# Optimization experiments

Hardware: AMD Instinct MI355X
Metric: run time of the kernel (lower is better)

The kernel has to match this reference:

```python
import jax, jax.numpy as jnp
import numpy as np

HIDDEN = 768
INTER = 2048
N_EXPERTS = 8
TOP_K = 2
SWIGLU_LIMIT = 7.0
N_TOK = 8192


def setup_inputs() -> dict:
    key = jax.random.key(0)
    k_x, k_r, k_gu, k_d = jax.random.split(key, 4)
    x = jax.random.normal(k_x, (N_TOK, HIDDEN), dtype=jnp.float32)
    router_w = jax.random.normal(k_r, (N_EXPERTS, HIDDEN), dtype=jnp.float32) * 0.02
    gate_up_proj = jax.random.normal(k_gu, (N_EXPERTS, 2 * INTER, HIDDEN), dtype=jnp.float32) * 0.02
    down_proj = jax.random.normal(k_d, (N_EXPERTS, HIDDEN, INTER), dtype=jnp.float32) * 0.02
    return {"x": x, "router_w": router_w, "gate_up_proj": gate_up_proj, "down_proj": down_proj}


def reference(x, router_w, gate_up_proj, down_proj):
    # router: [n_tok, E]
    router_logits = x @ router_w.T
    topk_vals, topk_idx = jax.lax.top_k(router_logits, TOP_K)  # [n_tok, k]
    topk_weights = jax.nn.softmax(topk_vals.astype(jnp.float32), axis=-1).astype(x.dtype)

    out = jnp.zeros_like(x)
    # Loop over the small fixed expert set; each expert is a dense GEMM over all
    # tokens, masked by its per-token routing weight (0 for unrouted tokens) —
    # identical math to the original gather/GEMM/scatter dispatch.
    for e in range(N_EXPERTS):
        # per-token weight for expert e (sums slots; each expert appears at most once per token)
        w_e = jnp.sum(jnp.where(topk_idx == e, topk_weights, 0.0), axis=-1)  # [n_tok]
        gate_up = x @ gate_up_proj[e].T  # [n_tok, 2*I]
        gate, up = jnp.split(gate_up, 2, axis=-1)
        up = jnp.minimum(up, SWIGLU_LIMIT)
        mlp_out = (jax.nn.silu(gate) * up) @ down_proj[e].T  # [n_tok, H]
        out = out + mlp_out * w_e[:, None]
    return out
```

## Files before the change

### kernel.cpp

```cpp
#include <hip/hip_runtime.h>
#include <hip/hip_bf16.h>

typedef unsigned short u16;
typedef unsigned int u32;
typedef short bf16x8 __attribute__((ext_vector_type(8)));
typedef float f32x4 __attribute__((ext_vector_type(4)));

#define NTOK 8192
#define HID 768
#define INTER 2048
#define NEXP 8

#define MFMA16(a, b, c) __builtin_amdgcn_mfma_f32_16x16x32_bf16(a, b, c, 0, 0, 0)
#define S_BARRIER() __builtin_amdgcn_s_barrier()
#define SETPRIO(x) __builtin_amdgcn_s_setprio(x)
#define WAITVM(n) asm volatile("s_waitcnt vmcnt(" #n ")" ::: "memory")

__device__ __forceinline__ u16 f2bf(float f) {
    u32 u = __builtin_bit_cast(u32, f);
    u32 r = (u + 0x7FFFu + ((u >> 16) & 1u)) >> 16;
    return (u16)r;
}

__device__ __forceinline__ void gld16(const void* g, void* l) {
    __builtin_amdgcn_global_load_lds((const __attribute__((address_space(1))) void*)g,
                                     (__attribute__((address_space(3))) void*)l, 16, 0, 0);
}

__global__ __launch_bounds__(256) void zero_kernel(float4* out4, int n4) {
    int i = blockIdx.x * blockDim.x + threadIdx.x;
    float4 z = {0.f, 0.f, 0.f, 0.f};
    int stride = gridDim.x * blockDim.x;
    for (int k = i; k < n4; k += stride) out4[k] = z;
}

__global__ __launch_bounds__(256) void cvt_kernel(const float* __restrict__ src, u16* __restrict__ dst, int n8) {
    int i = blockIdx.x * blockDim.x + threadIdx.x;
    int stride = gridDim.x * blockDim.x;
    for (; i < n8; i += stride) {
        const float4* s = (const float4*)(src + (size_t)i * 8);
        float4 a = s[0], b = s[1];
        u16 r[8] = {f2bf(a.x), f2bf(a.y), f2bf(a.z), f2bf(a.w),
                    f2bf(b.x), f2bf(b.y), f2bf(b.z), f2bf(b.w)};
        *(uint4*)(dst + (size_t)i * 8) = *(const uint4*)r;
    }
}

__global__ __launch_bounds__(256) void router2(const float* __restrict__ x, const float* __restrict__ rw,
                                               u32* __restrict__ route, float* __restrict__ wslot) {
    int wv = threadIdx.x >> 6, ln = threadIdx.x & 63;
    int t = blockIdx.x * 4 + wv;
    if (t >= NTOK) return;
    float xr[12];
#pragma unroll
    for (int j = 0; j < 12; j++) xr[j] = x[(size_t)t * HID + ln + j * 64];
    float lg[NEXP];
#pragma unroll
    for (int e = 0; e < NEXP; e++) {
        float a = 0.f;
#pragma unroll
        for (int j = 0; j < 12; j++) a += xr[j] * rw[e * HID + ln + j * 64];
#pragma unroll
        for (int off = 32; off; off >>= 1) a += __shfl_xor(a, off);
        lg[e] = a;
    }
    int i0 = 0;
    float v0 = lg[0];
#pragma unroll
    for (int e = 1; e < NEXP; e++)
        if (lg[e] > v0) { v0 = lg[e]; i0 = e; }
    int i1 = -1;
    float v1 = -1e30f;
#pragma unroll
    for (int e = 0; e < NEXP; e++) {
        if (e == i0) continue;
        if (lg[e] > v1) { v1 = lg[e]; i1 = e; }
    }
    float w0 = 1.f / (1.f + __expf(v1 - v0));
    float w1 = 1.f - w0;
    if (ln == 0) {
        wslot[0 * NTOK + t] = w0;
        wslot[1 * NTOK + t] = w1;
        route[t] = (u32)i0 | ((u32)i1 << 8);
    }
}

__global__ __launch_bounds__(1024) void scatter_kernel(const u32* __restrict__ route, int* __restrict__ counts,
                                                       int* __restrict__ tokslot, int* __restrict__ ntiles,
                                                       int* __restrict__ tiledesc) {
    __shared__ int sc[NEXP][1024];
    int tid = threadIdx.x;
    u32 rt[8];
    int cnt[NEXP] = {0, 0, 0, 0, 0, 0, 0, 0};
#pragma unroll
    for (int k = 0; k < 8; k++) {
        rt[k] = route[tid * 8 + k];
        cnt[rt[k] & 255]++;
        cnt[(rt[k] >> 8) & 255]++;
    }
#pragma unroll
    for (int e = 0; e < NEXP; e++) sc[e][tid] = cnt[e];
    __syncthreads();
    for (int off = 1; off < 1024; off <<= 1) {
        int v[NEXP];
#pragma unroll
        for (int e = 0; e < NEXP; e++) v[e] = (tid >= off) ? sc[e][tid - off] : 0;
        __syncthreads();
#pragma unroll
        for (int e = 0; e < NEXP; e++)
            if (tid >= off) sc[e][tid] += v[e];
        __syncthreads();
    }
    int base[NEXP];
#pragma unroll
    for (int e = 0; e < NEXP; e++) base[e] = sc[e][tid] - cnt[e];
#pragma unroll
    for (int k = 0; k < 8; k++) {
        int t = tid * 8 + k;
        int e0 = rt[k] & 255, e1 = (rt[k] >> 8) & 255;
        tokslot[e0 * NTOK + base[e0]] = t;
        base[e0]++;
        tokslot[e1 * NTOK + base[e1]] = t | (1 << 16);
        base[e1]++;
    }
    if (tid == 0) {
        int tot = 0;
        for (int e = 0; e < NEXP; e++) {
            int c = sc[e][1023];
            counts[e] = c;
            int nt = (c + 255) >> 8;
            for (int q = 0; q < nt; q++) tiledesc[tot++] = (e << 8) | q;
        }
        ntiles[0] = tot;
    }
}


#define QOFF(d, ab, kh) ((d)*65536 + (ab)*32768 + (kh)*16384)

#define STAGE(qo, p0, p1, ko)                        \
    do {                                             \
        char* dst_ = lds + (qo) + tid * 16;          \
        gld16((p0) + (ko), dst_);                    \
        gld16((p1) + (ko), dst_ + 8192);             \
    } while (0)

#define RD_A(d, kh, mh)                                                   \
    do {                                                                  \
        const char* Ab_ = lds + QOFF(d, 0, kh) + aOff;                    \
        af[0] = *(const bf16x8*)(Ab_ + ((mh)*4 + 0) * 1024);              \
        af[1] = *(const bf16x8*)(Ab_ + ((mh)*4 + 1) * 1024);              \
        af[2] = *(const bf16x8*)(Ab_ + ((mh)*4 + 2) * 1024);              \
        af[3] = *(const bf16x8*)(Ab_ + ((mh)*4 + 3) * 1024);              \
    } while (0)

#define RD_B(d, kh)                                                       \
    do {                                                                  \
        const char* Bb_ = lds + QOFF(d, 1, kh) + bOff;                    \
        bf[0] = *(const bf16x8*)(Bb_ + 0 * 1024);                         \
        bf[1] = *(const bf16x8*)(Bb_ + 1 * 1024);                         \
        bf[2] = *(const bf16x8*)(Bb_ + 2 * 1024);                         \
        bf[3] = *(const bf16x8*)(Bb_ + 3 * 1024);                         \
    } while (0)

#define MM(mh)                                                            \
    do {                                                                  \
        _Pragma("unroll") for (int m_ = 0; m_ < 4; m_++)                  \
            _Pragma("unroll") for (int n_ = 0; n_ < 4; n_++)              \
                acc[(mh)*4 + m_][n_] = MFMA16(af[m_], bf[n_], acc[(mh)*4 + m_][n_]); \
    } while (0)

#define PHASE_PAIR(dR, khR, qoE, pE0, pE1, koE, qoO, pO0, pO1, koO)       \
    do {                                                                  \
        bf16x8 af[4], bf[4];                                              \
        RD_A(dR, khR, 0);                                                 \
        RD_B(dR, khR);                                                    \
        STAGE(qoE, pE0, pE1, koE);                                        \
        S_BARRIER();                                                      \
        SETPRIO(1); MM(0); SETPRIO(0);                                    \
        S_BARRIER();                                                      \
        RD_A(dR, khR, 1);                                                 \
        STAGE(qoO, pO0, pO1, koO);                                        \
        WAITVM(8);                                                        \
        S_BARRIER();                                                      \
        SETPRIO(1); MM(1); SETPRIO(0);                                    \
        S_BARRIER();                                                      \
    } while (0)

#define PIPE8(NKT)                                                        \
    f32x4 acc[8][4];                                                      \
    _Pragma("unroll") for (int m_ = 0; m_ < 8; m_++)                      \
        _Pragma("unroll") for (int n_ = 0; n_ < 4; n_++) acc[m_][n_] = (f32x4)0.f; \
    int aOff = (wr * 128 + rsel) * 64 + ((g4 ^ (rsel & 3)) << 4);         \
    int bOff = (wc * 64 + rsel) * 64 + ((g4 ^ (rsel & 3)) << 4);          \
    STAGE(QOFF(0, 0, 0), aP0, aP1, 0);                                    \
    STAGE(QOFF(0, 1, 0), bP0, bP1, 0);                                    \
    STAGE(QOFF(0, 0, 1), aP0, aP1, 64);                                   \
    STAGE(QOFF(0, 1, 1), bP0, bP1, 64);                                   \
    STAGE(QOFF(1, 0, 0), aP0, aP1, 128);                                  \
    STAGE(QOFF(1, 1, 0), bP0, bP1, 128);                                  \
    WAITVM(8);                                                            \
    S_BARRIER();                                                          \
    for (int j = 0; j < (NKT) / 2; ++j) {                                 \
        int t1k = (2 * j + 1) * 128 + 64;                                 \
        int t2 = 2 * j + 2; if (t2 >= (NKT)) t2 = 0;                      \
        int t3 = 2 * j + 3; if (t3 >= (NKT)) t3 = 1;                      \
        int t2k0 = t2 * 128, t2k1 = t2 * 128 + 64, t3k0 = t3 * 128;       \
        PHASE_PAIR(0, 0, QOFF(1, 0, 1), aP0, aP1, t1k, QOFF(1, 1, 1), bP0, bP1, t1k);   \
        PHASE_PAIR(0, 1, QOFF(0, 0, 0), aP0, aP1, t2k0, QOFF(0, 1, 0), bP0, bP1, t2k0); \
        PHASE_PAIR(1, 0, QOFF(0, 0, 1), aP0, aP1, t2k1, QOFF(0, 1, 1), bP0, bP1, t2k1); \
        PHASE_PAIR(1, 1, QOFF(1, 0, 0), aP0, aP1, t3k0, QOFF(1, 1, 0), bP0, bP1, t3k0); \
    }                                                                     \
    WAITVM(0);                                                            \
    S_BARRIER();

__global__ __launch_bounds__(512, 2) void gateup8p(const u16* __restrict__ xb, const u16* __restrict__ gub,
                                                   const int* __restrict__ counts,
                                                   const int* __restrict__ ntiles, const int* __restrict__ tiledesc,
                                                   const int* __restrict__ tokslot, u16* __restrict__ h) {
    if ((int)blockIdx.x >= ntiles[0]) return;
    int td = tiledesc[blockIdx.x];
    int e = td >> 8;
    int cnt = counts[e];
    int row0 = (td & 255) * 256;
    int c0 = blockIdx.y * 128;

    extern __shared__ char lds[];
    int tid = threadIdx.x;
    int wv = tid >> 6, ln = tid & 63;
    int wr = wv >> 2, wc = wv & 3;
    int rsel = ln & 15, g4 = ln >> 4;

    int srow = tid >> 2, sl = tid & 3;
    int sx = ((sl ^ (srow & 3)) << 4);
    const char* aP0;
    const char* aP1;
    const char* bP0;
    const char* bP1;
    {
        int gr0 = row0 + srow; gr0 = gr0 < cnt ? gr0 : cnt - 1;
        int gr1 = row0 + 128 + srow; gr1 = gr1 < cnt ? gr1 : cnt - 1;
        int t0 = tokslot[e * NTOK + gr0] & 0xFFFF;
        int t1 = tokslot[e * NTOK + gr1] & 0xFFFF;
        aP0 = (const char*)xb + (size_t)t0 * (HID * 2) + sx;
        aP1 = (const char*)xb + (size_t)t1 * (HID * 2) + sx;
        int r0 = srow, r1 = 128 + srow;
        int wi0 = r0 & 63, wi1 = r1 & 63;
        int b0 = (wi0 >> 5) * 2048 + c0 + (r0 >> 6) * 32 + (wi0 & 31);
        int b1 = (wi1 >> 5) * 2048 + c0 + (r1 >> 6) * 32 + (wi1 & 31);
        bP0 = (const char*)gub + ((size_t)e * 4096 + b0) * (HID * 2) + sx;
        bP1 = (const char*)gub + ((size_t)e * 4096 + b1) * (HID * 2) + sx;
    }

    PIPE8(HID / 64)

#pragma unroll
    for (int mg = 0; mg < 8; mg++) {
#pragma unroll
        for (int j = 0; j < 4; j++) {
            int gr = row0 + wr * 128 + mg * 16 + g4 * 4 + j;
            if (gr >= cnt) continue;
            int ts = tokslot[e * NTOK + gr];
            int tok = ts & 0xFFFF, slot = ts >> 16;
            u16* hrow = h + (size_t)(slot * NTOK + tok) * INTER;
#pragma unroll
            for (int n = 0; n < 2; n++) {
                float gv = acc[mg][n][j];
                float uv = fminf(acc[mg][n + 2][j], 7.0f);
                float sg = gv / (1.0f + __expf(-gv));
                hrow[c0 + wc * 32 + n * 16 + rsel] = f2bf(sg * uv);
            }
        }
    }
}

__global__ __launch_bounds__(512, 2) void down8p(const u16* __restrict__ hb, const u16* __restrict__ dnb,
                                                 const int* __restrict__ counts,
                                                 const int* __restrict__ ntiles, const int* __restrict__ tiledesc,
                                                 const int* __restrict__ tokslot,
                                                 const float* __restrict__ wslot, float* __restrict__ out) {
    if ((int)blockIdx.x >= ntiles[0]) return;
    int td = tiledesc[blockIdx.x];
    int e = td >> 8;
    int cnt = counts[e];
    int row0 = (td & 255) * 256;
    int col0 = blockIdx.y * 256;

    extern __shared__ char lds[];
    int tid = threadIdx.x;
    int wv = tid >> 6, ln = tid & 63;
    int wr = wv >> 2, wc = wv & 3;
    int rsel = ln & 15, g4 = ln >> 4;

    int srow = tid >> 2, sl = tid & 3;
    int sx = ((sl ^ (srow & 3)) << 4);
    const char* aP0;
    const char* aP1;
    const char* bP0;
    const char* bP1;
    {
        int gr0 = row0 + srow; gr0 = gr0 < cnt ? gr0 : cnt - 1;
        int gr1 = row0 + 128 + srow; gr1 = gr1 < cnt ? gr1 : cnt - 1;
        int ts0 = tokslot[e * NTOK + gr0];
        int ts1 = tokslot[e * NTOK + gr1];
        aP0 = (const char*)hb + (size_t)((ts0 >> 16) * NTOK + (ts0 & 0xFFFF)) * (INTER * 2) + sx;
        aP1 = (const char*)hb + (size_t)((ts1 >> 16) * NTOK + (ts1 & 0xFFFF)) * (INTER * 2) + sx;
        bP0 = (const char*)dnb + ((size_t)e * HID + col0 + srow) * (INTER * 2) + sx;
        bP1 = (const char*)dnb + ((size_t)e * HID + col0 + 128 + srow) * (INTER * 2) + sx;
    }

    PIPE8(INTER / 64)

#pragma unroll
    for (int mg = 0; mg < 8; mg++) {
#pragma unroll
        for (int j = 0; j < 4; j++) {
            int gr = row0 + wr * 128 + mg * 16 + g4 * 4 + j;
            if (gr >= cnt) continue;
            int ts = tokslot[e * NTOK + gr];
            int tok = ts & 0xFFFF, slot = ts >> 16;
            float w = wslot[slot * NTOK + tok];
#pragma unroll
            for (int n = 0; n < 4; n++) {
                int col = col0 + wc * 64 + n * 16 + rsel;
                atomicAdd(&out[(size_t)tok * HID + col], w * acc[mg][n][j]);
            }
        }
    }
}

extern "C" void kernel_launch(void* const* d_in, const int* in_sizes, int n_in,
                              void* d_out, int out_size, void* d_ws, size_t ws_size,
                              hipStream_t stream) {
    const float* x = (const float*)d_in[0];
    const float* rw = (const float*)d_in[1];
    const float* gu = (const float*)d_in[2];
    const float* dn = (const float*)d_in[3];
    float* out = (float*)d_out;
    char* ws = (char*)d_ws;

    int* counts = (int*)(ws + 0);
    int* ntiles = (int*)(ws + 64);
    int* tiledesc = (int*)(ws + 128);
    int* tokslot = (int*)(ws + 512);
    float* wslot = (float*)(ws + 262656);
    u16* xb = (u16*)(ws + 328192);
    u16* gub = (u16*)(ws + 12911104);
    u16* dnb = (u16*)(ws + 63242752);
    u16* hb = (u16*)(ws + 88408576);
    u32* route = (u32*)(ws + 88408576);

    zero_kernel<<<1024, 256, 0, stream>>>((float4*)out, NTOK * HID / 4);
    cvt_kernel<<<2048, 256, 0, stream>>>(x, xb, NTOK * HID / 8);
    cvt_kernel<<<2048, 256, 0, stream>>>(gu, gub, NEXP * 2 * INTER * HID / 8);
    cvt_kernel<<<2048, 256, 0, stream>>>(dn, dnb, NEXP * HID * INTER / 8);
    router2<<<NTOK / 4, 256, 0, stream>>>(x, rw, route, wslot);
    scatter_kernel<<<1, 1024, 0, stream>>>(route, counts, tokslot, ntiles, tiledesc);
    gateup8p<<<dim3(72, 16), 512, 131072, stream>>>(xb, gub, counts, ntiles, tiledesc, tokslot, hb);
    down8p<<<dim3(72, 3), 512, 131072, stream>>>(hb, dnb, counts, ntiles, tiledesc, tokslot, wslot, out);
}
```

Before: 332.3 us.

## Replace 8-phase interleaved GEMM pipeline with simple double-buffered K=64 tiles

Swaps the finely interleaved 8-phase pipeline, which staged 32-wide K halves with multiple barriers per phase, for a plain two-buffer loop over 64-wide K tiles. Each iteration prefetches the next tile with eight 16-byte loads per thread, reads all A and B fragments for two K sub-steps, and issues 32 MFMAs per sub-step. It then waits for all loads and synchronises once. This cuts barrier count and index arithmetic. In exchange the load latency is only hidden by one tile of compute, since the full vmcnt(0) wait comes before the next iteration, and more fragment registers are live at once.

```diff
diff --git a/kernel.cpp b/kernel.cpp
--- a/kernel.cpp
+++ b/kernel.cpp
@@ -136,85 +136,58 @@
 }
 
 
-#define QOFF(d, ab, kh) ((d)*65536 + (ab)*32768 + (kh)*16384)
-
-#define STAGE(qo, p0, p1, ko)                        \
-    do {                                             \
-        char* dst_ = lds + (qo) + tid * 16;          \
-        gld16((p0) + (ko), dst_);                    \
-        gld16((p1) + (ko), dst_ + 8192);             \
+#define STAGE8(d, kt)                                        \
+    do {                                                     \
+        char* dA_ = lds + (d)*65536 + tid * 16;              \
+        char* dB_ = dA_ + 32768;                             \
+        size_t ko_ = (size_t)(kt)*128;                       \
+        gld16(aP[0] + ko_, dA_);                             \
+        gld16(aP[1] + ko_, dA_ + 8192);                      \
+        gld16(aP[2] + ko_, dA_ + 16384);                     \
+        gld16(aP[3] + ko_, dA_ + 24576);                     \
+        gld16(bP[0] + ko_, dB_);                             \
+        gld16(bP[1] + ko_, dB_ + 8192);                      \
+        gld16(bP[2] + ko_, dB_ + 16384);                     \
+        gld16(bP[3] + ko_, dB_ + 24576);                     \
     } while (0)
 
-#define RD_A(d, kh, mh)                                                   \
+#define MMALL()                                                           \
     do {                                                                  \
-        const char* Ab_ = lds + QOFF(d, 0, kh) + aOff;                    \
-        af[0] = *(const bf16x8*)(Ab_ + ((mh)*4 + 0) * 1024);              \
-        af[1] = *(const bf16x8*)(Ab_ + ((mh)*4 + 1) * 1024);              \
-        af[2] = *(const bf16x8*)(Ab_ + ((mh)*4 + 2) * 1024);              \
-        af[3] = *(const bf16x8*)(Ab_ + ((mh)*4 + 3) * 1024);              \
+        _Pragma("unroll") for (int m_ = 0; m_ < 8; m_++)                  \
+            _Pragma("unroll") for (int n_ = 0; n_ < 4; n_++)              \
+                acc[m_][n_] = MFMA16(af[m_], bfr[n_], acc[m_][n_]);       \
     } while (0)
 
-#define RD_B(d, kh)                                                       \
-    do {                                                                  \
-        const char* Bb_ = lds + QOFF(d, 1, kh) + bOff;                    \
-        bf[0] = *(const bf16x8*)(Bb_ + 0 * 1024);                         \
-        bf[1] = *(const bf16x8*)(Bb_ + 1 * 1024);                         \
-        bf[2] = *(const bf16x8*)(Bb_ + 2 * 1024);                         \
-        bf[3] = *(const bf16x8*)(Bb_ + 3 * 1024);                         \
-    } while (0)
-
-#define MM(mh)                                                            \
-    do {                                                                  \
-        _Pragma("unroll") for (int m_ = 0; m_ < 4; m_++)                  \
-            _Pragma("unroll") for (int n_ = 0; n_ < 4; n_++)              \
-                acc[(mh)*4 + m_][n_] = MFMA16(af[m_], bf[n_], acc[(mh)*4 + m_][n_]); \
-    } while (0)
-
-#define PHASE_PAIR(dR, khR, qoE, pE0, pE1, koE, qoO, pO0, pO1, koO)       \
-    do {                                                                  \
-        bf16x8 af[4], bf[4];                                              \
-        RD_A(dR, khR, 0);                                                 \
-        RD_B(dR, khR);                                                    \
-        STAGE(qoE, pE0, pE1, koE);                                        \
-        S_BARRIER();                                                      \
-        SETPRIO(1); MM(0); SETPRIO(0);                                    \
-        S_BARRIER();                                                      \
-        RD_A(dR, khR, 1);                                                 \
-        STAGE(qoO, pO0, pO1, koO);                                        \
-        WAITVM(8);                                                        \
-        S_BARRIER();                                                      \
-        SETPRIO(1); MM(1); SETPRIO(0);                                    \
-        S_BARRIER();                                                      \
-    } while (0)
-
-#define PIPE8(NKT)                                                        \
+#define PIPE2(NKT)                                                        \
     f32x4 acc[8][4];                                                      \
     _Pragma("unroll") for (int m_ = 0; m_ < 8; m_++)                      \
         _Pragma("unroll") for (int n_ = 0; n_ < 4; n_++) acc[m_][n_] = (f32x4)0.f; \
-    int aOff = (wr * 128 + rsel) * 64 + ((g4 ^ (rsel & 3)) << 4);         \
-    int bOff = (wc * 64 + rsel) * 64 + ((g4 ^ (rsel & 3)) << 4);          \
-    STAGE(QOFF(0, 0, 0), aP0, aP1, 0);                                    \
-    STAGE(QOFF(0, 1, 0), bP0, bP1, 0);                                    \
-    STAGE(QOFF(0, 0, 1), aP0, aP1, 64);                                   \
-    STAGE(QOFF(0, 1, 1), bP0, bP1, 64);                                   \
-    STAGE(QOFF(1, 0, 0), aP0, aP1, 128);                                  \
-    STAGE(QOFF(1, 1, 0), bP0, bP1, 128);                                  \
-    WAITVM(8);                                                            \
+    const int aBase = (wr * 128 + rsel) * 128;                            \
+    const int bBase = 32768 + (wc * 64 + rsel) * 128;                     \
+    const int s0 = ((g4 ^ (rsel & 7)) << 4);                              \
+    const int s1 = (((4 + g4) ^ (rsel & 7)) << 4);                        \
+    STAGE8(0, 0);                                                         \
+    WAITVM(0);                                                            \
     S_BARRIER();                                                          \
-    for (int j = 0; j < (NKT) / 2; ++j) {                                 \
-        int t1k = (2 * j + 1) * 128 + 64;                                 \
-        int t2 = 2 * j + 2; if (t2 >= (NKT)) t2 = 0;                      \
-        int t3 = 2 * j + 3; if (t3 >= (NKT)) t3 = 1;                      \
-        int t2k0 = t2 * 128, t2k1 = t2 * 128 + 64, t3k0 = t3 * 128;       \
-        PHASE_PAIR(0, 0, QOFF(1, 0, 1), aP0, aP1, t1k, QOFF(1, 1, 1), bP0, bP1, t1k);   \
-        PHASE_PAIR(0, 1, QOFF(0, 0, 0), aP0, aP1, t2k0, QOFF(0, 1, 0), bP0, bP1, t2k0); \
-        PHASE_PAIR(1, 0, QOFF(0, 0, 1), aP0, aP1, t2k1, QOFF(0, 1, 1), bP0, bP1, t2k1); \
-        PHASE_PAIR(1, 1, QOFF(1, 0, 0), aP0, aP1, t3k0, QOFF(1, 1, 0), bP0, bP1, t3k0); \
-    }                                                                     \
-    WAITVM(0);                                                            \
-    S_BARRIER();
-
-__global__ __launch_bounds__(512, 2) void gateup8p(const u16* __restrict__ xb, const u16* __restrict__ gub,
+    for (int t = 0; t < (NKT); ++t) {                                     \
+        if (t + 1 < (NKT)) STAGE8((t + 1) & 1, t + 1);                    \
+        const char* Tb = lds + (t & 1) * 65536;                           \
+        bf16x8 af[8], bfr[4];                                             \
+        _Pragma("unroll") for (int m_ = 0; m_ < 8; m_++)                  \
+            af[m_] = *(const bf16x8*)(Tb + aBase + m_ * 2048 + s0);       \
+        _Pragma("unroll") for (int n_ = 0; n_ < 4; n_++)                  \
+            bfr[n_] = *(const bf16x8*)(Tb + bBase + n_ * 2048 + s0);      \
+        SETPRIO(1); MMALL(); SETPRIO(0);                                  \
+        _Pragma("unroll") for (int m_ = 0; m_ < 8; m_++)                  \
+            af[m_] = *(const bf16x8*)(Tb + aBase + m_ * 2048 + s1);       \
+        _Pragma("unroll") for (int n_ = 0; n_ < 4; n_++)                  \
+            bfr[n_] = *(const bf16x8*)(Tb + bBase + n_ * 2048 + s1);      \
+        SETPRIO(1); MMALL(); SETPRIO(0);                                  \
+        WAITVM(0);                                                        \
+        S_BARRIER();                                                      \
+    }
+
+__global__ __launch_bounds__(512, 2) void gateup2p(const u16* __restrict__ xb, const u16* __restrict__ gub,
                                                    const int* __restrict__ counts,
                                                    const int* __restrict__ ntiles, const int* __restrict__ tiledesc,
                                                    const int* __restrict__ tokslot, u16* __restrict__ h) {
@@ -231,28 +204,23 @@
     int wr = wv >> 2, wc = wv & 3;
     int rsel = ln & 15, g4 = ln >> 4;
 
-    int srow = tid >> 2, sl = tid & 3;
-    int sx = ((sl ^ (srow & 3)) << 4);
-    const char* aP0;
-    const char* aP1;
-    const char* bP0;
-    const char* bP1;
-    {
-        int gr0 = row0 + srow; gr0 = gr0 < cnt ? gr0 : cnt - 1;
-        int gr1 = row0 + 128 + srow; gr1 = gr1 < cnt ? gr1 : cnt - 1;
-        int t0 = tokslot[e * NTOK + gr0] & 0xFFFF;
-        int t1 = tokslot[e * NTOK + gr1] & 0xFFFF;
-        aP0 = (const char*)xb + (size_t)t0 * (HID * 2) + sx;
-        aP1 = (const char*)xb + (size_t)t1 * (HID * 2) + sx;
-        int r0 = srow, r1 = 128 + srow;
-        int wi0 = r0 & 63, wi1 = r1 & 63;
-        int b0 = (wi0 >> 5) * 2048 + c0 + (r0 >> 6) * 32 + (wi0 & 31);
-        int b1 = (wi1 >> 5) * 2048 + c0 + (r1 >> 6) * 32 + (wi1 & 31);
-        bP0 = (const char*)gub + ((size_t)e * 4096 + b0) * (HID * 2) + sx;
-        bP1 = (const char*)gub + ((size_t)e * 4096 + b1) * (HID * 2) + sx;
-    }
-
-    PIPE8(HID / 64)
+    int srow = tid >> 3;
+    int sswz = ((tid & 7) ^ (srow & 7)) << 4;
+    const char* aP[4];
+    const char* bP[4];
+#pragma unroll
+    for (int c = 0; c < 4; c++) {
+        int r = c * 64 + srow;
+        int gr = row0 + r;
+        gr = gr < cnt ? gr : cnt - 1;
+        int tok = tokslot[e * NTOK + gr] & 0xFFFF;
+        aP[c] = (const char*)xb + (size_t)tok * (HID * 2) + sswz;
+        int wi = r & 63;
+        int b = (wi >> 5) * 2048 + c0 + (r >> 6) * 32 + (wi & 31);
+        bP[c] = (const char*)gub + ((size_t)e * 4096 + b) * (HID * 2) + sswz;
+    }
+
+    PIPE2(HID / 64)
 
 #pragma unroll
     for (int mg = 0; mg < 8; mg++) {
@@ -274,7 +242,7 @@
     }
 }
 
-__global__ __launch_bounds__(512, 2) void down8p(const u16* __restrict__ hb, const u16* __restrict__ dnb,
+__global__ __launch_bounds__(512, 2) void down2p(const u16* __restrict__ hb, const u16* __restrict__ dnb,
                                                  const int* __restrict__ counts,
                                                  const int* __restrict__ ntiles, const int* __restrict__ tiledesc,
                                                  const int* __restrict__ tokslot,
@@ -292,24 +260,21 @@
     int wr = wv >> 2, wc = wv & 3;
     int rsel = ln & 15, g4 = ln >> 4;
 
-    int srow = tid >> 2, sl = tid & 3;
-    int sx = ((sl ^ (srow & 3)) << 4);
-    const char* aP0;
-    const char* aP1;
-    const char* bP0;
-    const char* bP1;
-    {
-        int gr0 = row0 + srow; gr0 = gr0 < cnt ? gr0 : cnt - 1;
-        int gr1 = row0 + 128 + srow; gr1 = gr1 < cnt ? gr1 : cnt - 1;
-        int ts0 = tokslot[e * NTOK + gr0];
-        int ts1 = tokslot[e * NTOK + gr1];
-        aP0 = (const char*)hb + (size_t)((ts0 >> 16) * NTOK + (ts0 & 0xFFFF)) * (INTER * 2) + sx;
-        aP1 = (const char*)hb + (size_t)((ts1 >> 16) * NTOK + (ts1 & 0xFFFF)) * (INTER * 2) + sx;
-        bP0 = (const char*)dnb + ((size_t)e * HID + col0 + srow) * (INTER * 2) + sx;
-        bP1 = (const char*)dnb + ((size_t)e * HID + col0 + 128 + srow) * (INTER * 2) + sx;
-    }
-
-    PIPE8(INTER / 64)
+    int srow = tid >> 3;
+    int sswz = ((tid & 7) ^ (srow & 7)) << 4;
+    const char* aP[4];
+    const char* bP[4];
+#pragma unroll
+    for (int c = 0; c < 4; c++) {
+        int r = c * 64 + srow;
+        int gr = row0 + r;
+        gr = gr < cnt ? gr : cnt - 1;
+        int ts = tokslot[e * NTOK + gr];
+        aP[c] = (const char*)hb + (size_t)((ts >> 16) * NTOK + (ts & 0xFFFF)) * (INTER * 2) + sswz;
+        bP[c] = (const char*)dnb + ((size_t)e * HID + col0 + r) * (INTER * 2) + sswz;
+    }
+
+    PIPE2(INTER / 64)
 
 #pragma unroll
     for (int mg = 0; mg < 8; mg++) {
@@ -356,6 +321,6 @@
     cvt_kernel<<<2048, 256, 0, stream>>>(dn, dnb, NEXP * HID * INTER / 8);
     router2<<<NTOK / 4, 256, 0, stream>>>(x, rw, route, wslot);
     scatter_kernel<<<1, 1024, 0, stream>>>(route, counts, tokslot, ntiles, tiledesc);
-    gateup8p<<<dim3(72, 16), 512, 131072, stream>>>(xb, gub, counts, ntiles, tiledesc, tokslot, hb);
-    down8p<<<dim3(72, 3), 512, 131072, stream>>>(hb, dnb, counts, ntiles, tiledesc, tokslot, wslot, out);
-}
+    gateup2p<<<dim3(72, 16), 512, 131072, stream>>>(xb, gub, counts, ntiles, tiledesc, tokslot, hb);
+    down2p<<<dim3(72, 3), 512, 131072, stream>>>(hb, dnb, counts, ntiles, tiledesc, tokslot, wslot, out);
+}
```

Measured after the change: 315.4 us. -5.1%, faster.
